# Kernel tuning notes

Hardware: AMD Instinct MI355X
Metric: run time of the kernel (lower is better)

The kernel has to match this reference:

```python
import jax, jax.numpy as jnp
import numpy as np

N_HEADS = 32
N_KV_HEADS = 8
HEAD_DIM = 64  # dim // n_heads = 2048 // 32

def setup_inputs() -> dict:
    key = jax.random.key(0)
    k1, k2, k3, k4, k5 = jax.random.split(key, 5)
    B, T, D = 2, 2048, 2048
    s = 0.02
    return {
        "x": jax.random.normal(k1, (B, T, D), dtype=jnp.float32),
        "wq": jax.random.normal(k2, (D, D), dtype=jnp.float32) * s,
        "wk": jax.random.normal(k3, (N_KV_HEADS * HEAD_DIM, D), dtype=jnp.float32) * s,
        "wv": jax.random.normal(k4, (N_KV_HEADS * HEAD_DIM, D), dtype=jnp.float32) * s,
        "wo": jax.random.normal(k5, (D, D), dtype=jnp.float32) * s,
    }

def reference(x, wq, wk, wv, wo):
    B, T, D = x.shape
    ratio = N_HEADS // N_KV_HEADS
    scale = HEAD_DIM ** -0.5
    # projections (nn.Linear: x @ W.T)
    q = (x @ wq.T).reshape(B, T, N_HEADS, HEAD_DIM)
    k = (x @ wk.T).reshape(B, T, N_KV_HEADS, HEAD_DIM)
    v = (x @ wv.T).reshape(B, T, N_KV_HEADS, HEAD_DIM)
    # GQA expand: [B,T,kvh,d] -> [B,T,kvh*ratio,d]
    k = jnp.broadcast_to(k[:, :, :, None, :], (B, T, N_KV_HEADS, ratio, HEAD_DIM)).reshape(B, T, N_HEADS, HEAD_DIM)
    v = jnp.broadcast_to(v[:, :, :, None, :], (B, T, N_KV_HEADS, ratio, HEAD_DIM)).reshape(B, T, N_HEADS, HEAD_DIM)
    # [B,H,T,d]
    q = q.transpose(0, 2, 1, 3)
    k = k.transpose(0, 2, 1, 3)
    v = v.transpose(0, 2, 1, 3)
    # naive full score matrix [B,H,T,T]
    score = jnp.einsum('bhqd,bhkd->bhqk', q, k) * scale
    causal = jnp.triu(jnp.full((T, T), -jnp.inf, dtype=score.dtype), k=1)
    score = score + causal
    # upcast to fp32 for softmax (matches score.float())
    attn = jax.nn.softmax(score.astype(jnp.float32), axis=-1)
    out = jnp.einsum('bhqk,bhkd->bhqd', attn, v.astype(jnp.float32)).astype(x.dtype)
    out = out.transpose(0, 2, 1, 3).reshape(B, T, N_HEADS * HEAD_DIM)
    return out @ wo.T
```

## Files before the change

### kernel.cpp

```cpp
#include <hip/hip_runtime.h>
#include <hip/hip_bf16.h>

typedef unsigned short u16;
typedef unsigned int   u32;
typedef __attribute__((ext_vector_type(8))) short s16x8;
typedef __attribute__((ext_vector_type(4))) float f32x4;

__device__ __forceinline__ u16 f2bf(float f) {
    u32 u = __float_as_uint(f);
    u += 0x7fff + ((u >> 16) & 1);
    return (u16)(u >> 16);
}

__device__ __forceinline__ u16 f2bf_fast(float f) {
    __hip_bfloat16 h = __float2bfloat16(f);
    return *reinterpret_cast<u16*>(&h);
}

__device__ __forceinline__ f32x4 mfma16(s16x8 a, s16x8 b, f32x4 c) {
    return __builtin_amdgcn_mfma_f32_16x16x32_bf16(a, b, c, 0, 0, 0);
}

#define GLL16(g, l)                                                            \
    __builtin_amdgcn_global_load_lds(                                          \
        (const __attribute__((address_space(1))) void*)(g),                    \
        (__attribute__((address_space(3))) void*)(l), 16, 0, 0)

__global__ void cvt_f32_bf16(const float* __restrict__ src, u16* __restrict__ dst, int n8) {
    int i = blockIdx.x * blockDim.x + threadIdx.x;
    if (i >= n8) return;
    const float4* s4 = reinterpret_cast<const float4*>(src);
    float4 a = s4[2 * i], b = s4[2 * i + 1];
    s16x8 o;
    o[0] = (short)f2bf(a.x); o[1] = (short)f2bf(a.y);
    o[2] = (short)f2bf(a.z); o[3] = (short)f2bf(a.w);
    o[4] = (short)f2bf(b.x); o[5] = (short)f2bf(b.y);
    o[6] = (short)f2bf(b.z); o[7] = (short)f2bf(b.w);
    reinterpret_cast<s16x8*>(dst)[i] = o;
}

__global__ void cvt_weights(const float* __restrict__ wq, const float* __restrict__ wk,
                            const float* __restrict__ wv, const float* __restrict__ wo,
                            u16* __restrict__ wqkv, u16* __restrict__ wob) {
    int i = blockIdx.x * blockDim.x + threadIdx.x;
    const float* src; u16* dst;
    if (i < 524288)       { src = wq + (size_t)i * 8;            dst = wqkv + (size_t)i * 8; }
    else if (i < 655360)  { int j = i - 524288; src = wk + (size_t)j * 8; dst = wqkv + 4194304 + (size_t)j * 8; }
    else if (i < 786432)  { int j = i - 655360; src = wv + (size_t)j * 8; dst = wqkv + 5242880 + (size_t)j * 8; }
    else                  { int j = i - 786432; src = wo + (size_t)j * 8; dst = wob + (size_t)j * 8; }
    const float4* s4 = reinterpret_cast<const float4*>(src);
    float4 a = s4[0], b = s4[1];
    s16x8 o;
    o[0] = (short)f2bf(a.x); o[1] = (short)f2bf(a.y);
    o[2] = (short)f2bf(a.z); o[3] = (short)f2bf(a.w);
    o[4] = (short)f2bf(b.x); o[5] = (short)f2bf(b.y);
    o[6] = (short)f2bf(b.z); o[7] = (short)f2bf(b.w);
    *reinterpret_cast<s16x8*>(dst) = o;
}

template <int BF16_OUT>
__global__ __launch_bounds__(256, 2)
void gemm_bt(const u16* __restrict__ A, const u16* __restrict__ B,
             void* __restrict__ Cout, int M, int N, int K) {
    __shared__ __align__(16) u16 As[128 * 32];
    __shared__ __align__(16) u16 Bs[128 * 32];
    const int tid = threadIdx.x;
    const int w = tid >> 6, ln = tid & 63;
    const int m0 = blockIdx.y * 128, n0 = blockIdx.x * 128;
    const int wr = w >> 1, wc = w & 1;
    const int g = ln >> 4, c15 = ln & 15;
    f32x4 acc[4][4] = {};
    const int srow0 = w * 32 + (ln >> 2);
    const int spos = ln & 3;
    for (int k0 = 0; k0 < K; k0 += 32) {
        __syncthreads();
#pragma unroll
        for (int j = 0; j < 2; ++j) {
            int row = srow0 + j * 16;
            int ch = spos ^ ((row >> 1) & 3);
            const u16* ga = A + (size_t)(m0 + row) * K + k0 + ch * 8;
            GLL16(ga, (char*)As + (w * 32 + j * 16) * 64);
            const u16* gb = B + (size_t)(n0 + row) * K + k0 + ch * 8;
            GLL16(gb, (char*)Bs + (w * 32 + j * 16) * 64);
        }
        __syncthreads();
        s16x8 af[4], bfr[4];
#pragma unroll
        for (int ms = 0; ms < 4; ++ms) {
            int row = wr * 64 + ms * 16 + c15;
            int cp = g ^ ((row >> 1) & 3);
            af[ms] = *reinterpret_cast<const s16x8*>((const char*)As + row * 64 + cp * 16);
        }
#pragma unroll
        for (int ns = 0; ns < 4; ++ns) {
            int row = wc * 64 + ns * 16 + c15;
            int cp = g ^ ((row >> 1) & 3);
            bfr[ns] = *reinterpret_cast<const s16x8*>((const char*)Bs + row * 64 + cp * 16);
        }
        __builtin_amdgcn_s_setprio(1);
#pragma unroll
        for (int ms = 0; ms < 4; ++ms)
#pragma unroll
            for (int ns = 0; ns < 4; ++ns)
                acc[ms][ns] = mfma16(af[ms], bfr[ns], acc[ms][ns]);
        __builtin_amdgcn_s_setprio(0);
    }
#pragma unroll
    for (int ms = 0; ms < 4; ++ms)
#pragma unroll
        for (int ns = 0; ns < 4; ++ns)
#pragma unroll
            for (int r = 0; r < 4; ++r) {
                int row = m0 + wr * 64 + ms * 16 + g * 4 + r;
                int col = n0 + wc * 64 + ns * 16 + c15;
                float v = acc[ms][ns][r];
                if (BF16_OUT)
                    ((u16*)Cout)[(size_t)row * N + col] = f2bf(v);
                else
                    ((float*)Cout)[(size_t)row * N + col] = v;
            }
}

__global__ __launch_bounds__(256, 2)
void attn_fwd(const u16* __restrict__ qkv, u16* __restrict__ outp) {
    const int T = 2048, RS = 3072;
    const int pr = blockIdx.x, kvh = blockIdx.y, b = blockIdx.z;
    const int tid = threadIdx.x, w = tid >> 6, ln = tid & 63;
    const int g = ln >> 4, c15 = ln & 15;
    const int h = kvh * 4 + w;
    __shared__ __align__(16) u16 Ks[128 * 64];
    __shared__ __align__(16) u16 Vt[64 * 136];
    __shared__ __align__(16) u16 Ps[4][32 * 72];
    const size_t base = (size_t)b * T * RS;
    const float SCALE2 = 0.125f * 1.44269504088896f;
    const float THR = 8.0f;

    for (int ph = 0; ph < 2; ++ph) {
        const int qt = ph ? (63 - pr) : pr;
        const int qg0 = qt * 32;

        s16x8 qf[2][2];
#pragma unroll
        for (int ms = 0; ms < 2; ++ms)
#pragma unroll
            for (int ks = 0; ks < 2; ++ks)
                qf[ms][ks] = *reinterpret_cast<const s16x8*>(
                    qkv + base + (size_t)(qg0 + ms * 16 + c15) * RS + h * 64 + ks * 32 + g * 8);

        f32x4 o[2][4] = {};
        float mrow[2][4], lrow[2][4];
#pragma unroll
        for (int ms = 0; ms < 2; ++ms)
#pragma unroll
            for (int r = 0; r < 4; ++r) { mrow[ms][r] = -INFINITY; lrow[ms][r] = 0.f; }

        const int nt = (qt >> 2) + 1;
        for (int t = 0; t < nt; ++t) {
            __syncthreads();
#pragma unroll
            for (int j = 0; j < 4; ++j) {
                int row = w * 32 + j * 8 + (ln >> 3);
                int ch = (ln & 7) ^ (row & 7);
                const u16* gk = qkv + base + (size_t)(t * 128 + row) * RS + 2048 + kvh * 64 + ch * 8;
                GLL16(gk, (char*)Ks + (w * 32 + j * 8) * 128);
            }
#pragma unroll
            for (int j = 0; j < 4; ++j) {
                int cid = tid + j * 256;
                int kv = cid & 127, dch = cid >> 7;
                s16x8 vv = *reinterpret_cast<const s16x8*>(
                    qkv + base + (size_t)(t * 128 + kv) * RS + 2560 + kvh * 64 + dch * 8);
#pragma unroll
                for (int i = 0; i < 8; ++i)
                    Vt[(dch * 8 + i) * 136 + kv] = (u16)vv[i];
            }
            __syncthreads();

            f32x4 s[2][8] = {};
#pragma unroll
            for (int ks = 0; ks < 2; ++ks)
#pragma unroll
                for (int nh = 0; nh < 2; ++nh) {
                    s16x8 kf[4];
#pragma unroll
                    for (int n4 = 0; n4 < 4; ++n4) {
                        int row = (nh * 4 + n4) * 16 + c15;
                        int ch = (ks * 4 + g) ^ (row & 7);
                        kf[n4] = *reinterpret_cast<const s16x8*>((const char*)Ks + row * 128 + ch * 16);
                    }
                    __builtin_amdgcn_s_setprio(1);
#pragma unroll
                    for (int ms = 0; ms < 2; ++ms)
#pragma unroll
                        for (int n4 = 0; n4 < 4; ++n4)
                            s[ms][nh * 4 + n4] = mfma16(qf[ms][ks], kf[n4], s[ms][nh * 4 + n4]);
                    __builtin_amdgcn_s_setprio(0);
                }

            const bool lastT = (t == nt - 1);
            float mx2[2][4];
#pragma unroll
            for (int ms = 0; ms < 2; ++ms)
#pragma unroll
                for (int r = 0; r < 4; ++r) {
                    float mx = -INFINITY;
                    if (lastT) {
                        int qrow = qg0 + ms * 16 + g * 4 + r;
#pragma unroll
                        for (int ns = 0; ns < 8; ++ns) {
                            int col = t * 128 + ns * 16 + c15;
                            float v = s[ms][ns][r] * SCALE2;
                            v = (col <= qrow) ? v : -INFINITY;
                            s[ms][ns][r] = v;
                            mx = fmaxf(mx, v);
                        }
                    } else {
#pragma unroll
                        for (int ns = 0; ns < 8; ++ns) {
                            float v = s[ms][ns][r] * SCALE2;
                            s[ms][ns][r] = v;
                            mx = fmaxf(mx, v);
                        }
                    }
                    mx = fmaxf(mx, __shfl_xor(mx, 1));
                    mx = fmaxf(mx, __shfl_xor(mx, 2));
                    mx = fmaxf(mx, __shfl_xor(mx, 4));
                    mx = fmaxf(mx, __shfl_xor(mx, 8));
                    mx2[ms][r] = mx;
                }

            float growth = -INFINITY;
#pragma unroll
            for (int ms = 0; ms < 2; ++ms)
#pragma unroll
                for (int r = 0; r < 4; ++r)
                    growth = fmaxf(growth, mx2[ms][r] - mrow[ms][r]);
            if (__any(growth > THR)) {
#pragma unroll
                for (int ms = 0; ms < 2; ++ms)
#pragma unroll
                    for (int r = 0; r < 4; ++r) {
                        float mnew = fmaxf(mrow[ms][r], mx2[ms][r]);
                        float fac = exp2f(mrow[ms][r] - mnew);
                        mrow[ms][r] = mnew;
                        lrow[ms][r] *= fac;
#pragma unroll
                        for (int ds = 0; ds < 4; ++ds) o[ms][ds][r] *= fac;
                    }
            }

#pragma unroll
            for (int ms = 0; ms < 2; ++ms)
#pragma unroll
                for (int r = 0; r < 4; ++r) {
                    float m = mrow[ms][r];
                    float rs = 0.f;
#pragma unroll
                    for (int ns = 0; ns < 8; ++ns) {
                        float p = exp2f(s[ms][ns][r] - m);
                        s[ms][ns][r] = p;
                        rs += p;
                    }
                    lrow[ms][r] += rs;
                    int prow = ms * 16 + g * 4 + r;
#pragma unroll
                    for (int ns = 0; ns < 4; ++ns)
                        Ps[w][prow * 72 + ns * 16 + c15] = f2bf_fast(s[ms][ns][r]);
                }
#pragma unroll
            for (int ks = 0; ks < 2; ++ks) {
                s16x8 pf[2], vf[4];
#pragma unroll
                for (int ms = 0; ms < 2; ++ms)
                    pf[ms] = *reinterpret_cast<const s16x8*>(&Ps[w][(ms * 16 + c15) * 72 + ks * 32 + g * 8]);
#pragma unroll
                for (int ds = 0; ds < 4; ++ds)
                    vf[ds] = *reinterpret_cast<const s16x8*>(&Vt[(ds * 16 + c15) * 136 + ks * 32 + g * 8]);
                __builtin_amdgcn_s_setprio(1);
#pragma unroll
                for (int ms = 0; ms < 2; ++ms)
#pragma unroll
                    for (int ds = 0; ds < 4; ++ds)
                        o[ms][ds] = mfma16(pf[ms], vf[ds], o[ms][ds]);
                __builtin_amdgcn_s_setprio(0);
            }
#pragma unroll
            for (int ms = 0; ms < 2; ++ms)
#pragma unroll
                for (int r = 0; r < 4; ++r) {
                    int prow = ms * 16 + g * 4 + r;
#pragma unroll
                    for (int ns = 0; ns < 4; ++ns)
                        Ps[w][prow * 72 + ns * 16 + c15] = f2bf_fast(s[ms][ns + 4][r]);
                }
#pragma unroll
            for (int ks = 2; ks < 4; ++ks) {
                s16x8 pf[2], vf[4];
#pragma unroll
                for (int ms = 0; ms < 2; ++ms)
                    pf[ms] = *reinterpret_cast<const s16x8*>(&Ps[w][(ms * 16 + c15) * 72 + (ks - 2) * 32 + g * 8]);
#pragma unroll
                for (int ds = 0; ds < 4; ++ds)
                    vf[ds] = *reinterpret_cast<const s16x8*>(&Vt[(ds * 16 + c15) * 136 + ks * 32 + g * 8]);
                __builtin_amdgcn_s_setprio(1);
#pragma unroll
                for (int ms = 0; ms < 2; ++ms)
#pragma unroll
                    for (int ds = 0; ds < 4; ++ds)
                        o[ms][ds] = mfma16(pf[ms], vf[ds], o[ms][ds]);
                __builtin_amdgcn_s_setprio(0);
            }
        }

#pragma unroll
        for (int ms = 0; ms < 2; ++ms)
#pragma unroll
            for (int r = 0; r < 4; ++r) {
                float l = lrow[ms][r];
                l += __shfl_xor(l, 1);
                l += __shfl_xor(l, 2);
                l += __shfl_xor(l, 4);
                l += __shfl_xor(l, 8);
                float inv = 1.0f / l;
                int qrow = qg0 + ms * 16 + g * 4 + r;
#pragma unroll
                for (int ds = 0; ds < 4; ++ds)
                    outp[(size_t)(b * T + qrow) * 2048 + h * 64 + ds * 16 + c15] =
                        f2bf_fast(o[ms][ds][r] * inv);
            }
    }
}

extern "C" void kernel_launch(void* const* d_in, const int* in_sizes, int n_in,
                              void* d_out, int out_size, void* d_ws, size_t ws_size,
                              hipStream_t stream) {
    const float* x  = (const float*)d_in[0];
    const float* wq = (const float*)d_in[1];
    const float* wk = (const float*)d_in[2];
    const float* wv = (const float*)d_in[3];
    const float* wo = (const float*)d_in[4];

    u16* xb   = (u16*)d_ws;
    u16* wqkv = xb + 8388608;
    u16* wob  = wqkv + 6291456;
    u16* qkvb = wob + 4194304;
    u16* attb = qkvb + 12582912;

    cvt_f32_bf16<<<4096, 256, 0, stream>>>(x, xb, 1048576);
    cvt_weights<<<5120, 256, 0, stream>>>(wq, wk, wv, wo, wqkv, wob);

    gemm_bt<1><<<dim3(24, 32), 256, 0, stream>>>(xb, wqkv, qkvb, 4096, 3072, 2048);
    attn_fwd<<<dim3(32, 8, 2), 256, 0, stream>>>(qkvb, attb);
    gemm_bt<0><<<dim3(16, 32), 256, 0, stream>>>(attb, wob, d_out, 4096, 2048, 2048);
}
```

Measured before the change: 331.1 us.

## Split attention query tiles across 8 waves and swizzle grids for XCD locality

The attention kernel now runs 512 threads per block, with each wave handling 16 query rows of one head instead of 32. This halves per-wave register state and raises occupancy, and the K/V tile loads are shared across more waves. Both GEMMs and the attention kernel switch to 1D grids whose block indices are remapped so that neighbouring tiles land on the same XCD for better L2 reuse. The GEMM launch bound is also raised to 3 blocks per CU. The costs are more register pressure on the GEMM and more per-block synchronisation for attention.

```diff
diff --git a/kernel.cpp b/kernel.cpp
--- a/kernel.cpp
+++ b/kernel.cpp
@@ -59,14 +59,18 @@
 }
 
 template <int BF16_OUT>
-__global__ __launch_bounds__(256, 2)
+__global__ __launch_bounds__(256, 3)
 void gemm_bt(const u16* __restrict__ A, const u16* __restrict__ B,
-             void* __restrict__ Cout, int M, int N, int K) {
+             void* __restrict__ Cout, int M, int N, int K, int nbx) {
+    const int nwg = gridDim.x;
+    const int cpx = nwg >> 3;
+    const int swz = (blockIdx.x & 7) * cpx + (blockIdx.x >> 3);
+    const int by = swz / nbx, bx = swz - by * nbx;
     __shared__ __align__(16) u16 As[128 * 32];
     __shared__ __align__(16) u16 Bs[128 * 32];
     const int tid = threadIdx.x;
     const int w = tid >> 6, ln = tid & 63;
-    const int m0 = blockIdx.y * 128, n0 = blockIdx.x * 128;
+    const int m0 = by * 128, n0 = bx * 128;
     const int wr = w >> 1, wc = w & 1;
     const int g = ln >> 4, c15 = ln & 15;
     f32x4 acc[4][4] = {};
@@ -121,52 +125,50 @@
             }
 }
 
-__global__ __launch_bounds__(256, 2)
+__global__ __launch_bounds__(512, 4)
 void attn_fwd(const u16* __restrict__ qkv, u16* __restrict__ outp) {
     const int T = 2048, RS = 3072;
-    const int pr = blockIdx.x, kvh = blockIdx.y, b = blockIdx.z;
+    const int swz = (blockIdx.x & 7) * 64 + (blockIdx.x >> 3);
+    const int pr = swz & 31, kvh = (swz >> 5) & 7, b = swz >> 8;
     const int tid = threadIdx.x, w = tid >> 6, ln = tid & 63;
     const int g = ln >> 4, c15 = ln & 15;
-    const int h = kvh * 4 + w;
+    const int h = kvh * 4 + (w >> 1);
+    const int qs = w & 1;
     __shared__ __align__(16) u16 Ks[128 * 64];
     __shared__ __align__(16) u16 Vt[64 * 136];
-    __shared__ __align__(16) u16 Ps[4][32 * 72];
+    __shared__ __align__(16) u16 Ps[8][16 * 72];
     const size_t base = (size_t)b * T * RS;
     const float SCALE2 = 0.125f * 1.44269504088896f;
     const float THR = 8.0f;
 
     for (int ph = 0; ph < 2; ++ph) {
-        const int qt = ph ? (63 - pr) : pr;
-        const int qg0 = qt * 32;
-
-        s16x8 qf[2][2];
-#pragma unroll
-        for (int ms = 0; ms < 2; ++ms)
-#pragma unroll
-            for (int ks = 0; ks < 2; ++ks)
-                qf[ms][ks] = *reinterpret_cast<const s16x8*>(
-                    qkv + base + (size_t)(qg0 + ms * 16 + c15) * RS + h * 64 + ks * 32 + g * 8);
-
-        f32x4 o[2][4] = {};
-        float mrow[2][4], lrow[2][4];
-#pragma unroll
-        for (int ms = 0; ms < 2; ++ms)
-#pragma unroll
-            for (int r = 0; r < 4; ++r) { mrow[ms][r] = -INFINITY; lrow[ms][r] = 0.f; }
-
-        const int nt = (qt >> 2) + 1;
+        const int qb = ph ? (63 - pr) : pr;
+        const int qg0 = qb * 32 + qs * 16;
+
+        s16x8 qf[2];
+#pragma unroll
+        for (int ks = 0; ks < 2; ++ks)
+            qf[ks] = *reinterpret_cast<const s16x8*>(
+                qkv + base + (size_t)(qg0 + c15) * RS + h * 64 + ks * 32 + g * 8);
+
+        f32x4 o[4] = {};
+        float mrow[4], lrow[4];
+#pragma unroll
+        for (int r = 0; r < 4; ++r) { mrow[r] = -INFINITY; lrow[r] = 0.f; }
+
+        const int nt = (qb >> 2) + 1;
         for (int t = 0; t < nt; ++t) {
             __syncthreads();
 #pragma unroll
-            for (int j = 0; j < 4; ++j) {
-                int row = w * 32 + j * 8 + (ln >> 3);
+            for (int j = 0; j < 2; ++j) {
+                int row = j * 64 + w * 8 + (ln >> 3);
                 int ch = (ln & 7) ^ (row & 7);
                 const u16* gk = qkv + base + (size_t)(t * 128 + row) * RS + 2048 + kvh * 64 + ch * 8;
-                GLL16(gk, (char*)Ks + (w * 32 + j * 8) * 128);
-            }
-#pragma unroll
-            for (int j = 0; j < 4; ++j) {
-                int cid = tid + j * 256;
+                GLL16(gk, (char*)Ks + (j * 64 + w * 8) * 128);
+            }
+#pragma unroll
+            for (int j = 0; j < 2; ++j) {
+                int cid = tid + j * 512;
                 int kv = cid & 127, dch = cid >> 7;
                 s16x8 vv = *reinterpret_cast<const s16x8*>(
                     qkv + base + (size_t)(t * 128 + kv) * RS + 2560 + kvh * 64 + dch * 8);
@@ -176,7 +178,7 @@
             }
             __syncthreads();
 
-            f32x4 s[2][8] = {};
+            f32x4 s[8] = {};
 #pragma unroll
             for (int ks = 0; ks < 2; ++ks)
 #pragma unroll
@@ -190,144 +192,121 @@
                     }
                     __builtin_amdgcn_s_setprio(1);
 #pragma unroll
-                    for (int ms = 0; ms < 2; ++ms)
-#pragma unroll
-                        for (int n4 = 0; n4 < 4; ++n4)
-                            s[ms][nh * 4 + n4] = mfma16(qf[ms][ks], kf[n4], s[ms][nh * 4 + n4]);
+                    for (int n4 = 0; n4 < 4; ++n4)
+                        s[nh * 4 + n4] = mfma16(qf[ks], kf[n4], s[nh * 4 + n4]);
                     __builtin_amdgcn_s_setprio(0);
                 }
 
             const bool lastT = (t == nt - 1);
-            float mx2[2][4];
-#pragma unroll
-            for (int ms = 0; ms < 2; ++ms)
+            float mx2[4];
+#pragma unroll
+            for (int r = 0; r < 4; ++r) {
+                float mx = -INFINITY;
+                if (lastT) {
+                    int qrow = qg0 + g * 4 + r;
+#pragma unroll
+                    for (int ns = 0; ns < 8; ++ns) {
+                        int col = t * 128 + ns * 16 + c15;
+                        float v = s[ns][r] * SCALE2;
+                        v = (col <= qrow) ? v : -INFINITY;
+                        s[ns][r] = v;
+                        mx = fmaxf(mx, v);
+                    }
+                } else {
+#pragma unroll
+                    for (int ns = 0; ns < 8; ++ns) {
+                        float v = s[ns][r] * SCALE2;
+                        s[ns][r] = v;
+                        mx = fmaxf(mx, v);
+                    }
+                }
+                mx = fmaxf(mx, __shfl_xor(mx, 1));
+                mx = fmaxf(mx, __shfl_xor(mx, 2));
+                mx = fmaxf(mx, __shfl_xor(mx, 4));
+                mx = fmaxf(mx, __shfl_xor(mx, 8));
+                mx2[r] = mx;
+            }
+
+            float growth = -INFINITY;
+#pragma unroll
+            for (int r = 0; r < 4; ++r) growth = fmaxf(growth, mx2[r] - mrow[r]);
+            if (__any(growth > THR)) {
 #pragma unroll
                 for (int r = 0; r < 4; ++r) {
-                    float mx = -INFINITY;
-                    if (lastT) {
-                        int qrow = qg0 + ms * 16 + g * 4 + r;
-#pragma unroll
-                        for (int ns = 0; ns < 8; ++ns) {
-                            int col = t * 128 + ns * 16 + c15;
-                            float v = s[ms][ns][r] * SCALE2;
-                            v = (col <= qrow) ? v : -INFINITY;
-                            s[ms][ns][r] = v;
-                            mx = fmaxf(mx, v);
-                        }
-                    } else {
-#pragma unroll
-                        for (int ns = 0; ns < 8; ++ns) {
-                            float v = s[ms][ns][r] * SCALE2;
-                            s[ms][ns][r] = v;
-                            mx = fmaxf(mx, v);
-                        }
-                    }
-                    mx = fmaxf(mx, __shfl_xor(mx, 1));
-                    mx = fmaxf(mx, __shfl_xor(mx, 2));
-                    mx = fmaxf(mx, __shfl_xor(mx, 4));
-                    mx = fmaxf(mx, __shfl_xor(mx, 8));
-                    mx2[ms][r] = mx;
+                    float mnew = fmaxf(mrow[r], mx2[r]);
+                    float fac = exp2f(mrow[r] - mnew);
+                    mrow[r] = mnew;
+                    lrow[r] *= fac;
+#pragma unroll
+                    for (int ds = 0; ds < 4; ++ds) o[ds][r] *= fac;
                 }
-
-            float growth = -INFINITY;
-#pragma unroll
-            for (int ms = 0; ms < 2; ++ms)
-#pragma unroll
-                for (int r = 0; r < 4; ++r)
-                    growth = fmaxf(growth, mx2[ms][r] - mrow[ms][r]);
-            if (__any(growth > THR)) {
-#pragma unroll
-                for (int ms = 0; ms < 2; ++ms)
-#pragma unroll
-                    for (int r = 0; r < 4; ++r) {
-                        float mnew = fmaxf(mrow[ms][r], mx2[ms][r]);
-                        float fac = exp2f(mrow[ms][r] - mnew);
-                        mrow[ms][r] = mnew;
-                        lrow[ms][r] *= fac;
-#pragma unroll
-                        for (int ds = 0; ds < 4; ++ds) o[ms][ds][r] *= fac;
-                    }
-            }
-
-#pragma unroll
-            for (int ms = 0; ms < 2; ++ms)
-#pragma unroll
-                for (int r = 0; r < 4; ++r) {
-                    float m = mrow[ms][r];
-                    float rs = 0.f;
-#pragma unroll
-                    for (int ns = 0; ns < 8; ++ns) {
-                        float p = exp2f(s[ms][ns][r] - m);
-                        s[ms][ns][r] = p;
-                        rs += p;
-                    }
-                    lrow[ms][r] += rs;
-                    int prow = ms * 16 + g * 4 + r;
-#pragma unroll
-                    for (int ns = 0; ns < 4; ++ns)
-                        Ps[w][prow * 72 + ns * 16 + c15] = f2bf_fast(s[ms][ns][r]);
+            }
+
+#pragma unroll
+            for (int r = 0; r < 4; ++r) {
+                float m = mrow[r];
+                float rs = 0.f;
+#pragma unroll
+                for (int ns = 0; ns < 8; ++ns) {
+                    float p = exp2f(s[ns][r] - m);
+                    s[ns][r] = p;
+                    rs += p;
                 }
+                lrow[r] += rs;
+                int prow = g * 4 + r;
+#pragma unroll
+                for (int ns = 0; ns < 4; ++ns)
+                    Ps[w][prow * 72 + ns * 16 + c15] = f2bf_fast(s[ns][r]);
+            }
 #pragma unroll
             for (int ks = 0; ks < 2; ++ks) {
-                s16x8 pf[2], vf[4];
-#pragma unroll
-                for (int ms = 0; ms < 2; ++ms)
-                    pf[ms] = *reinterpret_cast<const s16x8*>(&Ps[w][(ms * 16 + c15) * 72 + ks * 32 + g * 8]);
+                s16x8 pf, vf[4];
+                pf = *reinterpret_cast<const s16x8*>(&Ps[w][c15 * 72 + ks * 32 + g * 8]);
 #pragma unroll
                 for (int ds = 0; ds < 4; ++ds)
                     vf[ds] = *reinterpret_cast<const s16x8*>(&Vt[(ds * 16 + c15) * 136 + ks * 32 + g * 8]);
                 __builtin_amdgcn_s_setprio(1);
 #pragma unroll
-                for (int ms = 0; ms < 2; ++ms)
-#pragma unroll
-                    for (int ds = 0; ds < 4; ++ds)
-                        o[ms][ds] = mfma16(pf[ms], vf[ds], o[ms][ds]);
+                for (int ds = 0; ds < 4; ++ds)
+                    o[ds] = mfma16(pf, vf[ds], o[ds]);
                 __builtin_amdgcn_s_setprio(0);
             }
 #pragma unroll
-            for (int ms = 0; ms < 2; ++ms)
-#pragma unroll
-                for (int r = 0; r < 4; ++r) {
-                    int prow = ms * 16 + g * 4 + r;
-#pragma unroll
-                    for (int ns = 0; ns < 4; ++ns)
-                        Ps[w][prow * 72 + ns * 16 + c15] = f2bf_fast(s[ms][ns + 4][r]);
-                }
+            for (int r = 0; r < 4; ++r) {
+                int prow = g * 4 + r;
+#pragma unroll
+                for (int ns = 0; ns < 4; ++ns)
+                    Ps[w][prow * 72 + ns * 16 + c15] = f2bf_fast(s[ns + 4][r]);
+            }
 #pragma unroll
             for (int ks = 2; ks < 4; ++ks) {
-                s16x8 pf[2], vf[4];
-#pragma unroll
-                for (int ms = 0; ms < 2; ++ms)
-                    pf[ms] = *reinterpret_cast<const s16x8*>(&Ps[w][(ms * 16 + c15) * 72 + (ks - 2) * 32 + g * 8]);
+                s16x8 pf, vf[4];
+                pf = *reinterpret_cast<const s16x8*>(&Ps[w][c15 * 72 + (ks - 2) * 32 + g * 8]);
 #pragma unroll
                 for (int ds = 0; ds < 4; ++ds)
                     vf[ds] = *reinterpret_cast<const s16x8*>(&Vt[(ds * 16 + c15) * 136 + ks * 32 + g * 8]);
                 __builtin_amdgcn_s_setprio(1);
 #pragma unroll
-                for (int ms = 0; ms < 2; ++ms)
-#pragma unroll
-                    for (int ds = 0; ds < 4; ++ds)
-                        o[ms][ds] = mfma16(pf[ms], vf[ds], o[ms][ds]);
+                for (int ds = 0; ds < 4; ++ds)
+                    o[ds] = mfma16(pf, vf[ds], o[ds]);
                 __builtin_amdgcn_s_setprio(0);
             }
         }
 
 #pragma unroll
-        for (int ms = 0; ms < 2; ++ms)
-#pragma unroll
-            for (int r = 0; r < 4; ++r) {
-                float l = lrow[ms][r];
-                l += __shfl_xor(l, 1);
-                l += __shfl_xor(l, 2);
-                l += __shfl_xor(l, 4);
-                l += __shfl_xor(l, 8);
-                float inv = 1.0f / l;
-                int qrow = qg0 + ms * 16 + g * 4 + r;
-#pragma unroll
-                for (int ds = 0; ds < 4; ++ds)
-                    outp[(size_t)(b * T + qrow) * 2048 + h * 64 + ds * 16 + c15] =
-                        f2bf_fast(o[ms][ds][r] * inv);
-            }
+        for (int r = 0; r < 4; ++r) {
+            float l = lrow[r];
+            l += __shfl_xor(l, 1);
+            l += __shfl_xor(l, 2);
+            l += __shfl_xor(l, 4);
+            l += __shfl_xor(l, 8);
+            float inv = 1.0f / l;
+            int qrow = qg0 + g * 4 + r;
+#pragma unroll
+            for (int ds = 0; ds < 4; ++ds)
+                outp[(size_t)(b * T + qrow) * 2048 + h * 64 + ds * 16 + c15] =
+                    f2bf_fast(o[ds][r] * inv);
+        }
     }
 }
 
@@ -349,7 +328,7 @@
     cvt_f32_bf16<<<4096, 256, 0, stream>>>(x, xb, 1048576);
     cvt_weights<<<5120, 256, 0, stream>>>(wq, wk, wv, wo, wqkv, wob);
 
-    gemm_bt<1><<<dim3(24, 32), 256, 0, stream>>>(xb, wqkv, qkvb, 4096, 3072, 2048);
-    attn_fwd<<<dim3(32, 8, 2), 256, 0, stream>>>(qkvb, attb);
-    gemm_bt<0><<<dim3(16, 32), 256, 0, stream>>>(attb, wob, d_out, 4096, 2048, 2048);
-}
+    gemm_bt<1><<<768, 256, 0, stream>>>(xb, wqkv, qkvb, 4096, 3072, 2048, 24);
+    attn_fwd<<<512, 512, 0, stream>>>(qkvb, attb);
+    gemm_bt<0><<<512, 256, 0, stream>>>(attb, wob, d_out, 4096, 2048, 2048, 16);
+}
```

Result: faster. 314.9 us (-4.9%).
